# Kernel optimization log

Hardware: AMD Instinct MI355X
Metric: run time of the kernel (lower is better)

Reference implementation:

```python
import jax, jax.numpy as jnp
import numpy as np

HEADS = 16
DIM_HEAD = 64
NPATCH = 256
LN_EPS = 1e-5


def setup_inputs() -> dict:
    key = jax.random.key(0)
    ks = jax.random.split(key, 6)
    B, S, D = 4, 2048, 1024
    inner = HEADS * DIM_HEAD  # 1024
    x = jax.random.normal(ks[0], (B, S, D), dtype=jnp.float32)
    ln_gamma = jnp.ones((D,), dtype=jnp.float32)
    ln_beta = jnp.zeros((D,), dtype=jnp.float32)
    # torch Linear: y = x @ W.T; we store the transposed weight directly.
    Wqkv = jax.random.normal(ks[1], (D, 3 * inner), dtype=jnp.float32) / np.sqrt(D)
    Wout = jax.random.normal(ks[2], (inner, D), dtype=jnp.float32) / np.sqrt(inner)
    bout = jnp.zeros((D,), dtype=jnp.float32)
    return {"x": x, "ln_gamma": ln_gamma, "ln_beta": ln_beta,
            "Wqkv": Wqkv, "Wout": Wout, "bout": bout}


def reference(x, ln_gamma, ln_beta, Wqkv, Wout, bout):
    B, S, D = x.shape
    # LayerNorm
    mu = jnp.mean(x, axis=-1, keepdims=True)
    var = jnp.mean(jnp.square(x - mu), axis=-1, keepdims=True)
    xn = (x - mu) * jax.lax.rsqrt(var + LN_EPS) * ln_gamma + ln_beta
    # QKV projection
    qkv = xn @ Wqkv  # [B, S, 3*H*Dh]
    q, k, v = jnp.split(qkv, 3, axis=-1)
    q = q.reshape(B, S, HEADS, DIM_HEAD)
    k = k.reshape(B, S, HEADS, DIM_HEAD)
    v = v.reshape(B, S, HEADS, DIM_HEAD)
    scale = DIM_HEAD ** -0.5
    dots = jnp.einsum('bqhd,bkhd->bhqk', q, k) * scale  # [B,H,S,S]
    # block-causal mask: query window i attends to key windows 0..i
    win = jnp.arange(S) // NPATCH
    mask = win[:, None] >= win[None, :]  # [S, S] bool
    dots = jnp.where(mask[None, None], dots, -jnp.inf)
    attn = jax.nn.softmax(dots, axis=-1)
    out = jnp.einsum('bhqk,bkhd->bqhd', attn, v).reshape(B, S, HEADS * DIM_HEAD)
    return out @ Wout + bout
```

## Files before the change

### kernel.cpp

```cpp
#include <hip/hip_runtime.h>
#include <stdint.h>

typedef unsigned short u16;
typedef __attribute__((ext_vector_type(8))) short bf16x8;
typedef __attribute__((ext_vector_type(4))) float f32x4;
typedef __attribute__((ext_vector_type(4))) unsigned short u16x4;
typedef __attribute__((ext_vector_type(4))) unsigned int u32x4;

#define DEVI static __device__ __forceinline__

#define QSCALE (0.125f * 1.4426950408889634f)

DEVI u16 f2bf(float f) {
  union { float f; unsigned int u; } v; v.f = f;
  unsigned int u = v.u + 0x7fffu + ((v.u >> 16) & 1u);
  return (u16)(u >> 16);
}
DEVI void gl16(const void* g, void* l) {
  __builtin_amdgcn_global_load_lds(
      (__attribute__((address_space(1))) void*)g,
      (__attribute__((address_space(3))) void*)l, 16, 0, 0);
}
DEVI unsigned int cvtpk(float a, float b) {
  unsigned int r;
  asm("v_cvt_pk_bf16_f32 %0, %1, %2" : "=v"(r) : "v"(a), "v"(b));
  return r;
}
DEVI float fexp2(float x) {
  float r;
  asm("v_exp_f32 %0, %1\n\ts_nop 0" : "=v"(r) : "v"(x));
  return r;
}
DEVI float fmax4(f32x4 v) {
  return fmaxf(fmaxf(v[0], v[1]), fmaxf(v[2], v[3]));
}

__global__ __launch_bounds__(256) void k_ln_split(
    const float* __restrict__ x, const float* __restrict__ gamma,
    const float* __restrict__ beta, u16* __restrict__ xh) {
  const int row = blockIdx.x;
  const int t = threadIdx.x;
  const float4* xr = (const float4*)(x + (size_t)row * 1024);
  float4 v = xr[t];
  float s = v.x + v.y + v.z + v.w;
  float s2 = v.x * v.x + v.y * v.y + v.z * v.z + v.w * v.w;
  #pragma unroll
  for (int m = 1; m < 64; m <<= 1) { s += __shfl_xor(s, m); s2 += __shfl_xor(s2, m); }
  __shared__ float ls[4], ls2[4];
  if ((t & 63) == 0) { ls[t >> 6] = s; ls2[t >> 6] = s2; }
  __syncthreads();
  s = ls[0] + ls[1] + ls[2] + ls[3];
  s2 = ls2[0] + ls2[1] + ls2[2] + ls2[3];
  float mu = s * (1.0f / 1024.0f);
  float var = s2 * (1.0f / 1024.0f) - mu * mu;
  float rstd = rsqrtf(var + 1e-5f);
  float4 g = ((const float4*)gamma)[t];
  float4 b = ((const float4*)beta)[t];
  float xv[4] = {v.x, v.y, v.z, v.w};
  float gg[4] = {g.x, g.y, g.z, g.w};
  float bb[4] = {b.x, b.y, b.z, b.w};
  u16x4 hv;
  #pragma unroll
  for (int i = 0; i < 4; i++) {
    float xn = (xv[i] - mu) * rstd * gg[i] + bb[i];
    hv[i] = f2bf(xn);
  }
  ((u16x4*)xh)[(size_t)row * 256 + t] = hv;
}

__global__ __launch_bounds__(256) void k_wsplit_t(
    const float* __restrict__ W, u16* __restrict__ Wth, int K, int N) {
  __shared__ float tile[32][33];
  const int t = threadIdx.x;
  const int tx = t & 31, ty = t >> 5;
  #pragma unroll
  for (int i = 0; i < 4; i++) {
    int k = blockIdx.y * 32 + ty + i * 8;
    int n = blockIdx.x * 32 + tx;
    tile[ty + i * 8][tx] = W[(size_t)k * N + n];
  }
  __syncthreads();
  #pragma unroll
  for (int i = 0; i < 4; i++) {
    int n = blockIdx.x * 32 + ty + i * 8;
    int k = blockIdx.y * 32 + tx;
    Wth[(size_t)n * K + k] = f2bf(tile[tx][ty + i * 8]);
  }
}

template <int MODE>
__global__ __launch_bounds__(256) void k_gemm(
    const u16* __restrict__ Ah, const u16* __restrict__ Bh,
    u16* __restrict__ Qh, u16* __restrict__ Kh, u16* __restrict__ Vth,
    float* __restrict__ Cout, const float* __restrict__ bias) {
  __shared__ u16 sA[2][128 * 64];
  __shared__ u16 sB[2][128 * 64];
  const int t = threadIdx.x, lane = t & 63, w = t >> 6;
  const int bm = blockIdx.x, bn = blockIdx.y;
  const int wm = (w >> 1) * 64, wn = (w & 1) * 64;
  const int g = lane >> 4, c = lane & 15;
  const size_t arow0 = (size_t)bm * 128, brow0 = (size_t)bn * 128;

  const int r0 = t >> 3, cc0 = t & 7;
  const int cs0 = cc0 ^ (r0 & 7);
  const u16* gA = Ah + (arow0 + r0) * 1024 + cs0 * 8;
  const u16* gB = Bh + (brow0 + r0) * 1024 + cs0 * 8;

  f32x4 acc[4][4] = {};

  #pragma unroll
  for (int i = 0; i < 4; i++) {
    gl16(gA + (size_t)i * 32768, sA[0] + (size_t)(t + i * 256) * 8);
    gl16(gB + (size_t)i * 32768, sB[0] + (size_t)(t + i * 256) * 8);
  }
  gA += 64; gB += 64;
  __syncthreads();

  for (int kt = 0; kt < 16; kt++) {
    const int cur = kt & 1, nxt = cur ^ 1;
    if (kt + 1 < 16) {
      #pragma unroll
      for (int i = 0; i < 4; i++) {
        gl16(gA + (size_t)i * 32768, sA[nxt] + (size_t)(t + i * 256) * 8);
        gl16(gB + (size_t)i * 32768, sB[nxt] + (size_t)(t + i * 256) * 8);
      }
      gA += 64; gB += 64;
    }
    #pragma unroll
    for (int ks = 0; ks < 2; ks++) {
      bf16x8 afh[4], bfh[4];
      #pragma unroll
      for (int mi = 0; mi < 4; mi++) {
        int row = wm + mi * 16 + c;
        afh[mi] = *(const bf16x8*)(sA[cur] + row * 64 + (((ks * 4 + g) ^ (row & 7)) * 8));
      }
      #pragma unroll
      for (int ni = 0; ni < 4; ni++) {
        int row = wn + ni * 16 + c;
        bfh[ni] = *(const bf16x8*)(sB[cur] + row * 64 + (((ks * 4 + g) ^ (row & 7)) * 8));
      }
      #pragma unroll
      for (int mi = 0; mi < 4; mi++)
        #pragma unroll
        for (int ni = 0; ni < 4; ni++)
          acc[mi][ni] = __builtin_amdgcn_mfma_f32_16x16x32_bf16(afh[mi], bfh[ni], acc[mi][ni], 0, 0, 0);
    }
    __syncthreads();
  }

  if (MODE == 0) {
    #pragma unroll
    for (int mi = 0; mi < 4; mi++) {
      int grow0 = bm * 128 + wm + mi * 16 + g * 4;
      int b = grow0 >> 11, s0 = grow0 & 2047;
      #pragma unroll
      for (int ni = 0; ni < 4; ni++) {
        int gcol = bn * 128 + wn + ni * 16 + c;
        int which = gcol >> 10, rem = gcol & 1023;
        int hh = rem >> 6, dd = rem & 63;
        if (which == 2) {
          u16x4 hv;
          #pragma unroll
          for (int r = 0; r < 4; r++) hv[r] = f2bf(acc[mi][ni][r]);
          size_t off = ((size_t)((b * 16 + hh) * 64 + dd)) * 2048 + s0;
          *(u16x4*)(Vth + off) = hv;
        } else {
          u16* dh = which ? Kh : Qh;
          float sc = which ? 1.0f : QSCALE;
          #pragma unroll
          for (int r = 0; r < 4; r++) {
            size_t off = ((size_t)(b * 16 + hh) * 2048 + (s0 + r)) * 64 + dd;
            dh[off] = f2bf(acc[mi][ni][r] * sc);
          }
        }
      }
    }
  } else {
    #pragma unroll
    for (int mi = 0; mi < 4; mi++) {
      int grow0 = bm * 128 + wm + mi * 16 + g * 4;
      #pragma unroll
      for (int ni = 0; ni < 4; ni++) {
        int gcol = bn * 128 + wn + ni * 16 + c;
        float bb = bias[gcol];
        #pragma unroll
        for (int r = 0; r < 4; r++)
          Cout[(size_t)(grow0 + r) * 1024 + gcol] = acc[mi][ni][r] + bb;
      }
    }
  }
}

__global__ __launch_bounds__(512, 4) void k_attn(
    const u16* __restrict__ Qh, const u16* __restrict__ Kh,
    const u16* __restrict__ Vth, u16* __restrict__ Oh) {
  __shared__ u16 lK[2][128 * 64], lV[2][64 * 128];
  const int t = threadIdx.x, lane = t & 63, w = t >> 6;
  const int bh = blockIdx.x;
  const int qt = 15 - blockIdx.y;
  const int b = bh >> 4, h = bh & 15;
  const int qrow0 = qt * 128;
  const int kvlen = (qt / 2 + 1) * 256;
  const int g = lane >> 4, c = lane & 15;

  bf16x8 qf[2];
  {
    const u16* qb = Qh + ((size_t)bh * 2048 + qrow0 + w * 16) * 64;
    #pragma unroll
    for (int ks = 0; ks < 2; ks++)
      qf[ks] = *(const bf16x8*)(qb + (size_t)c * 64 + ks * 32 + g * 8);
  }

  const u16* Kb = Kh + (size_t)bh * 2048 * 64;
  const u16* Vb = Vth + (size_t)bh * 64 * 2048;

  int kbase[2], vbase[4];
  #pragma unroll
  for (int ks = 0; ks < 2; ks++) kbase[ks] = c * 64 + (((ks * 4 + g) ^ (c & 7)) * 8);
  #pragma unroll
  for (int ks = 0; ks < 4; ks++) vbase[ks] = c * 128 + (((ks * 4 + g) ^ c) * 8);

  const int kr0 = t >> 3, kcs0 = (t & 7) ^ (kr0 & 7);
  const int vr0 = t >> 4, vcs0 = (t & 15) ^ (vr0 & 15);

  const bf16x8 vones = {(short)0x3F80, (short)0x3F80, (short)0x3F80, (short)0x3F80,
                        (short)0x3F80, (short)0x3F80, (short)0x3F80, (short)0x3F80};

  float mrun = 0.f;
  f32x4 lsum = {0.f, 0.f, 0.f, 0.f};
  f32x4 o[4] = {};

  const int ntiles = kvlen >> 7;

  gl16(Kb + (size_t)kr0 * 64 + kcs0 * 8, lK[0] + (size_t)t * 8);
  gl16(Kb + (size_t)(kr0 + 64) * 64 + kcs0 * 8, lK[0] + (size_t)(t + 512) * 8);
  gl16(Vb + (size_t)vr0 * 2048 + vcs0 * 8, lV[0] + (size_t)t * 8);
  gl16(Vb + (size_t)(vr0 + 32) * 2048 + vcs0 * 8, lV[0] + (size_t)(t + 512) * 8);
  __syncthreads();

  const u16* gK = Kb + (size_t)(128 + kr0) * 64 + kcs0 * 8;
  const u16* gV = Vb + (size_t)vr0 * 2048 + 128 + vcs0 * 8;

  for (int kt = 0; kt < ntiles; kt++) {
    const int cur = kt & 1, nxt = cur ^ 1;
    if (kt + 1 < ntiles) {
      gl16(gK, lK[nxt] + (size_t)t * 8);
      gl16(gK + 64 * 64, lK[nxt] + (size_t)(t + 512) * 8);
      gl16(gV, lV[nxt] + (size_t)t * 8);
      gl16(gV + 32 * 2048, lV[nxt] + (size_t)(t + 512) * 8);
      gK += 128 * 64;  gV += 128;
    }

    f32x4 s[8];
    #pragma unroll
    for (int ni = 0; ni < 8; ni++)
      s[ni] = (f32x4){-mrun, -mrun, -mrun, -mrun};
    __builtin_amdgcn_s_setprio(1);
    #pragma unroll
    for (int ni = 0; ni < 8; ni++)
      #pragma unroll
      for (int ks = 0; ks < 2; ks++) {
        bf16x8 kf = *(const bf16x8*)(lK[cur] + ni * 1024 + kbase[ks]);
        s[ni] = __builtin_amdgcn_mfma_f32_16x16x32_bf16(kf, qf[ks], s[ni], 0, 0, 0);
      }
    __builtin_amdgcn_s_setprio(0);

    float tl = fmaxf(fmaxf(fmaxf(fmax4(s[0]), fmax4(s[1])), fmaxf(fmax4(s[2]), fmax4(s[3]))),
                     fmaxf(fmaxf(fmax4(s[4]), fmax4(s[5])), fmaxf(fmax4(s[6]), fmax4(s[7]))));
    if (!__all(tl <= 8.0f)) {
      float tm = fmaxf(tl, __shfl_xor(tl, 16));
      tm = fmaxf(tm, __shfl_xor(tm, 32));
      float delta = fmaxf(tm, 0.0f);
      mrun += delta;
      float al = fexp2(-delta);
      #pragma unroll
      for (int ni = 0; ni < 8; ni++)
        #pragma unroll
        for (int r = 0; r < 4; r++) s[ni][r] -= delta;
      #pragma unroll
      for (int r = 0; r < 4; r++) {
        float ar = __shfl(al, g * 4 + r);
        lsum[r] *= ar;
        #pragma unroll
        for (int di = 0; di < 4; di++) o[di][r] *= ar;
      }
    }

    bf16x8 pa[4];
    #pragma unroll
    for (int ks = 0; ks < 4; ks++) {
      unsigned int e0 = cvtpk(fexp2(s[2 * ks][0]), fexp2(s[2 * ks][1]));
      unsigned int e1 = cvtpk(fexp2(s[2 * ks][2]), fexp2(s[2 * ks][3]));
      unsigned int f0 = cvtpk(fexp2(s[2 * ks + 1][0]), fexp2(s[2 * ks + 1][1]));
      unsigned int f1 = cvtpk(fexp2(s[2 * ks + 1][2]), fexp2(s[2 * ks + 1][3]));
      asm volatile("v_permlane32_swap_b32 %0, %1" : "+v"(e0), "+v"(f0));
      asm volatile("v_permlane16_swap_b32 %0, %1" : "+v"(e0), "+v"(f0));
      asm volatile("v_permlane32_swap_b32 %0, %1" : "+v"(e1), "+v"(f1));
      asm volatile("v_permlane16_swap_b32 %0, %1" : "+v"(e1), "+v"(f1));
      union { u32x4 u; bf16x8 bv; } cvu;
      cvu.u = (u32x4){e0, e1, f0, f1};
      pa[ks] = cvu.bv;
    }

    __builtin_amdgcn_s_setprio(1);
    #pragma unroll
    for (int di = 0; di < 4; di++)
      #pragma unroll
      for (int ks = 0; ks < 4; ks++) {
        bf16x8 vf = *(const bf16x8*)(lV[cur] + di * 2048 + vbase[ks]);
        o[di] = __builtin_amdgcn_mfma_f32_16x16x32_bf16(pa[ks], vf, o[di], 0, 0, 0);
      }
    #pragma unroll
    for (int ks = 0; ks < 4; ks++)
      lsum = __builtin_amdgcn_mfma_f32_16x16x32_bf16(pa[ks], vones, lsum, 0, 0, 0);
    __builtin_amdgcn_s_setprio(0);

    __syncthreads();
  }

  #pragma unroll
  for (int r = 0; r < 4; r++) {
    float ir = 1.0f / lsum[r];
    int srow = qrow0 + w * 16 + g * 4 + r;
    size_t rowo = ((size_t)b * 2048 + srow) * 1024 + h * 64;
    #pragma unroll
    for (int di = 0; di < 4; di++)
      Oh[rowo + di * 16 + c] = f2bf(o[di][r] * ir);
  }
}

extern "C" void kernel_launch(void* const* d_in, const int* in_sizes, int n_in,
                              void* d_out, int out_size, void* d_ws, size_t ws_size,
                              hipStream_t stream) {
  const float* x     = (const float*)d_in[0];
  const float* gamma = (const float*)d_in[1];
  const float* beta  = (const float*)d_in[2];
  const float* Wqkv  = (const float*)d_in[3];
  const float* Wout  = (const float*)d_in[4];
  const float* bout  = (const float*)d_in[5];
  float* out = (float*)d_out;

  char* ws = (char*)d_ws;
  size_t off = 0;
  auto alloc = [&](size_t bytes) { char* p = ws + off; off += (bytes + 255) & ~(size_t)255; return p; };
  const size_t SZ_XN = (size_t)8192 * 1024 * 2;
  const size_t SZ_WQ = (size_t)3072 * 1024 * 2;
  const size_t SZ_WO = (size_t)1024 * 1024 * 2;
  const size_t SZ_QKV = (size_t)4 * 16 * 2048 * 64 * 2;
  u16* xnh  = (u16*)alloc(SZ_XN);
  u16* wqth = (u16*)alloc(SZ_WQ);
  u16* woth = (u16*)alloc(SZ_WO);
  u16* Qh  = (u16*)alloc(SZ_QKV);
  u16* Kh  = (u16*)alloc(SZ_QKV);
  u16* Vth = (u16*)alloc(SZ_QKV);
  if (off > ws_size) return;

  k_ln_split<<<8192, 256, 0, stream>>>(x, gamma, beta, xnh);
  k_wsplit_t<<<dim3(96, 32), 256, 0, stream>>>(Wqkv, wqth, 1024, 3072);
  k_wsplit_t<<<dim3(32, 32), 256, 0, stream>>>(Wout, woth, 1024, 1024);
  k_gemm<0><<<dim3(64, 24), 256, 0, stream>>>(xnh, wqth,
                                              Qh, Kh, Vth, nullptr, nullptr);
  k_attn<<<dim3(64, 16), 512, 0, stream>>>(Qh, Kh, Vth, xnh);
  k_gemm<1><<<dim3(64, 8), 256, 0, stream>>>(xnh, woth,
                                             nullptr, nullptr, nullptr,
                                             out, bout);
}
```

Baseline: 164.0 us.

## Use 256x256 tiled, finely pipelined 8-wave GEMM for QKV projection

Replaces the templated 128x128 GEMM for the QKV projection with a dedicated kernel that computes a 256x256 tile using 512 threads (8 waves), each wave holding a 128x64 accumulator. The K loop is split into four sub-phases. Each phase interleaves LDS fragment loads, async global->LDS staging of the next half-tile, and partial vmcnt waits plus barriers, with setprio raised around the MFMA bursts. The goal is more data reuse per loaded tile and better overlap of memory with MFMA. The costs are higher register pressure, 128 KB of LDS per block, and fewer blocks in the grid (384), which may leave some CUs idle. The output projection keeps the old 128x128 kernel, now specialized.

```diff
diff --git a/kernel.cpp b/kernel.cpp
--- a/kernel.cpp
+++ b/kernel.cpp
@@ -88,10 +88,169 @@
   }
 }
 
-template <int MODE>
-__global__ __launch_bounds__(256) void k_gemm(
+__global__ __launch_bounds__(512, 2) void k_gemmq(
     const u16* __restrict__ Ah, const u16* __restrict__ Bh,
-    u16* __restrict__ Qh, u16* __restrict__ Kh, u16* __restrict__ Vth,
+    u16* __restrict__ Qh, u16* __restrict__ Kh, u16* __restrict__ Vth) {
+  __shared__ u16 sA[2][256 * 64];
+  __shared__ u16 sB[2][256 * 64];
+  const int t = threadIdx.x, lane = t & 63, w = t >> 6;
+  const int bm = blockIdx.x, bn = blockIdx.y;
+  const int wm2 = w >> 2, wn4 = w & 3;
+  const int g = lane >> 4, c = lane & 15;
+  const size_t arow0 = (size_t)bm * 256, brow0 = (size_t)bn * 256;
+
+  const int sr = t >> 3;
+  const int scs = (t & 7) ^ (sr & 7);
+  const int brs = (t >> 3) & 31;
+  const int bcs = (t & 7) ^ (brs & 7);
+  const int bsj = t >> 8;
+
+  f32x4 acc[8][4] = {};
+
+#define STAGE_A(u, kt, b) do { \
+    int rA0 = (u) * 64 + sr, rA1 = 128 + rA0; \
+    gl16(Ah + (arow0 + rA0) * 1024 + (size_t)(kt) * 64 + scs * 8, \
+         sA[b] + (size_t)((u) * 512 + t) * 8); \
+    gl16(Ah + (arow0 + rA1) * 1024 + (size_t)(kt) * 64 + scs * 8, \
+         sA[b] + (size_t)(1024 + (u) * 512 + t) * 8); \
+  } while (0)
+#define STAGE_B(u, kt, b) do { \
+    int s0_ = bsj, s1_ = bsj + 2; \
+    int rB0 = (u) * 32 + s0_ * 64 + brs, rB1 = (u) * 32 + s1_ * 64 + brs; \
+    gl16(Bh + (brow0 + rB0) * 1024 + (size_t)(kt) * 64 + bcs * 8, \
+         sB[b] + (size_t)(rB0 * 8 + (t & 7)) * 8); \
+    gl16(Bh + (brow0 + rB1) * 1024 + (size_t)(kt) * 64 + bcs * 8, \
+         sB[b] + (size_t)(rB1 * 8 + (t & 7)) * 8); \
+  } while (0)
+#define PWAIT(tail) do { \
+    if (tail) asm volatile("s_waitcnt vmcnt(0)" ::: "memory"); \
+    else      asm volatile("s_waitcnt vmcnt(6)" ::: "memory"); \
+    __builtin_amdgcn_s_barrier(); \
+    __builtin_amdgcn_sched_barrier(0); \
+  } while (0)
+
+  STAGE_A(0, 0, 0); STAGE_B(0, 0, 0);
+  STAGE_A(1, 0, 0); STAGE_B(1, 0, 0);
+  STAGE_A(0, 1, 1); STAGE_B(0, 1, 1);
+  PWAIT(0);
+
+  bf16x8 af[8], bf0[4], bf1[4];
+  for (int kt = 0; kt < 16; kt++) {
+    const int cur = kt & 1;
+    const int tail = (kt >= 14);
+    const u16* A_ = sA[cur];
+    const u16* B_ = sB[cur];
+
+    #pragma unroll
+    for (int mi = 0; mi < 4; mi++)
+      #pragma unroll
+      for (int ks = 0; ks < 2; ks++) {
+        int row = wm2 * 128 + mi * 16 + c;
+        af[mi * 2 + ks] = *(const bf16x8*)(A_ + row * 64 + (((ks * 4 + g) ^ (row & 7)) * 8));
+      }
+    #pragma unroll
+    for (int ni = 0; ni < 2; ni++)
+      #pragma unroll
+      for (int ks = 0; ks < 2; ks++) {
+        int row = wn4 * 64 + ni * 16 + c;
+        bf0[ni * 2 + ks] = *(const bf16x8*)(B_ + row * 64 + (((ks * 4 + g) ^ (row & 7)) * 8));
+      }
+    if (kt + 1 < 16) STAGE_A(1, kt + 1, (kt + 1) & 1);
+    PWAIT(tail);
+    __builtin_amdgcn_s_setprio(1);
+    #pragma unroll
+    for (int mi = 0; mi < 4; mi++)
+      #pragma unroll
+      for (int ni = 0; ni < 2; ni++)
+        #pragma unroll
+        for (int ks = 0; ks < 2; ks++)
+          acc[mi][ni] = __builtin_amdgcn_mfma_f32_16x16x32_bf16(af[mi * 2 + ks], bf0[ni * 2 + ks], acc[mi][ni], 0, 0, 0);
+    __builtin_amdgcn_s_setprio(0);
+
+    #pragma unroll
+    for (int ni = 0; ni < 2; ni++)
+      #pragma unroll
+      for (int ks = 0; ks < 2; ks++) {
+        int row = wn4 * 64 + 32 + ni * 16 + c;
+        bf1[ni * 2 + ks] = *(const bf16x8*)(B_ + row * 64 + (((ks * 4 + g) ^ (row & 7)) * 8));
+      }
+    if (kt + 1 < 16) STAGE_B(1, kt + 1, (kt + 1) & 1);
+    PWAIT(tail);
+    __builtin_amdgcn_s_setprio(1);
+    #pragma unroll
+    for (int mi = 0; mi < 4; mi++)
+      #pragma unroll
+      for (int ni = 0; ni < 2; ni++)
+        #pragma unroll
+        for (int ks = 0; ks < 2; ks++)
+          acc[mi][2 + ni] = __builtin_amdgcn_mfma_f32_16x16x32_bf16(af[mi * 2 + ks], bf1[ni * 2 + ks], acc[mi][2 + ni], 0, 0, 0);
+    __builtin_amdgcn_s_setprio(0);
+
+    #pragma unroll
+    for (int mi = 0; mi < 4; mi++)
+      #pragma unroll
+      for (int ks = 0; ks < 2; ks++) {
+        int row = wm2 * 128 + 64 + mi * 16 + c;
+        af[mi * 2 + ks] = *(const bf16x8*)(A_ + row * 64 + (((ks * 4 + g) ^ (row & 7)) * 8));
+      }
+    if (kt + 2 < 16) STAGE_A(0, kt + 2, cur);
+    PWAIT(tail);
+    __builtin_amdgcn_s_setprio(1);
+    #pragma unroll
+    for (int mi = 0; mi < 4; mi++)
+      #pragma unroll
+      for (int ni = 0; ni < 2; ni++)
+        #pragma unroll
+        for (int ks = 0; ks < 2; ks++)
+          acc[4 + mi][ni] = __builtin_amdgcn_mfma_f32_16x16x32_bf16(af[mi * 2 + ks], bf0[ni * 2 + ks], acc[4 + mi][ni], 0, 0, 0);
+    __builtin_amdgcn_s_setprio(0);
+
+    if (kt + 2 < 16) STAGE_B(0, kt + 2, cur);
+    PWAIT(tail);
+    __builtin_amdgcn_s_setprio(1);
+    #pragma unroll
+    for (int mi = 0; mi < 4; mi++)
+      #pragma unroll
+      for (int ni = 0; ni < 2; ni++)
+        #pragma unroll
+        for (int ks = 0; ks < 2; ks++)
+          acc[4 + mi][2 + ni] = __builtin_amdgcn_mfma_f32_16x16x32_bf16(af[mi * 2 + ks], bf1[ni * 2 + ks], acc[4 + mi][2 + ni], 0, 0, 0);
+    __builtin_amdgcn_s_setprio(0);
+  }
+
+  #pragma unroll
+  for (int am = 0; am < 8; am++) {
+    int grow0 = bm * 256 + wm2 * 128 + (am >> 2) * 64 + (am & 3) * 16 + g * 4;
+    int b = grow0 >> 11, s0 = grow0 & 2047;
+    #pragma unroll
+    for (int an = 0; an < 4; an++) {
+      int gcol = bn * 256 + wn4 * 64 + (an >> 1) * 32 + (an & 1) * 16 + c;
+      int which = gcol >> 10, rem = gcol & 1023;
+      int hh = rem >> 6, dd = rem & 63;
+      if (which == 2) {
+        u16x4 hv;
+        #pragma unroll
+        for (int r = 0; r < 4; r++) hv[r] = f2bf(acc[am][an][r]);
+        size_t off = ((size_t)((b * 16 + hh) * 64 + dd)) * 2048 + s0;
+        *(u16x4*)(Vth + off) = hv;
+      } else {
+        u16* dh = which ? Kh : Qh;
+        float sc = which ? 1.0f : QSCALE;
+        #pragma unroll
+        for (int r = 0; r < 4; r++) {
+          size_t off = ((size_t)(b * 16 + hh) * 2048 + (s0 + r)) * 64 + dd;
+          dh[off] = f2bf(acc[am][an][r] * sc);
+        }
+      }
+    }
+  }
+#undef STAGE_A
+#undef STAGE_B
+#undef PWAIT
+}
+
+__global__ __launch_bounds__(256) void k_gemmo(
+    const u16* __restrict__ Ah, const u16* __restrict__ Bh,
     float* __restrict__ Cout, const float* __restrict__ bias) {
   __shared__ u16 sA[2][128 * 64];
   __shared__ u16 sB[2][128 * 64];
@@ -148,45 +307,16 @@
     __syncthreads();
   }
 
-  if (MODE == 0) {
-    #pragma unroll
-    for (int mi = 0; mi < 4; mi++) {
-      int grow0 = bm * 128 + wm + mi * 16 + g * 4;
-      int b = grow0 >> 11, s0 = grow0 & 2047;
-      #pragma unroll
-      for (int ni = 0; ni < 4; ni++) {
-        int gcol = bn * 128 + wn + ni * 16 + c;
-        int which = gcol >> 10, rem = gcol & 1023;
-        int hh = rem >> 6, dd = rem & 63;
-        if (which == 2) {
-          u16x4 hv;
-          #pragma unroll
-          for (int r = 0; r < 4; r++) hv[r] = f2bf(acc[mi][ni][r]);
-          size_t off = ((size_t)((b * 16 + hh) * 64 + dd)) * 2048 + s0;
-          *(u16x4*)(Vth + off) = hv;
-        } else {
-          u16* dh = which ? Kh : Qh;
-          float sc = which ? 1.0f : QSCALE;
-          #pragma unroll
-          for (int r = 0; r < 4; r++) {
-            size_t off = ((size_t)(b * 16 + hh) * 2048 + (s0 + r)) * 64 + dd;
-            dh[off] = f2bf(acc[mi][ni][r] * sc);
-          }
-        }
-      }
-    }
-  } else {
-    #pragma unroll
-    for (int mi = 0; mi < 4; mi++) {
-      int grow0 = bm * 128 + wm + mi * 16 + g * 4;
-      #pragma unroll
-      for (int ni = 0; ni < 4; ni++) {
-        int gcol = bn * 128 + wn + ni * 16 + c;
-        float bb = bias[gcol];
-        #pragma unroll
-        for (int r = 0; r < 4; r++)
-          Cout[(size_t)(grow0 + r) * 1024 + gcol] = acc[mi][ni][r] + bb;
-      }
+  #pragma unroll
+  for (int mi = 0; mi < 4; mi++) {
+    int grow0 = bm * 128 + wm + mi * 16 + g * 4;
+    #pragma unroll
+    for (int ni = 0; ni < 4; ni++) {
+      int gcol = bn * 128 + wn + ni * 16 + c;
+      float bb = bias[gcol];
+      #pragma unroll
+      for (int r = 0; r < 4; r++)
+        Cout[(size_t)(grow0 + r) * 1024 + gcol] = acc[mi][ni][r] + bb;
     }
   }
 }
@@ -358,10 +488,7 @@
   k_ln_split<<<8192, 256, 0, stream>>>(x, gamma, beta, xnh);
   k_wsplit_t<<<dim3(96, 32), 256, 0, stream>>>(Wqkv, wqth, 1024, 3072);
   k_wsplit_t<<<dim3(32, 32), 256, 0, stream>>>(Wout, woth, 1024, 1024);
-  k_gemm<0><<<dim3(64, 24), 256, 0, stream>>>(xnh, wqth,
-                                              Qh, Kh, Vth, nullptr, nullptr);
+  k_gemmq<<<dim3(32, 12), 512, 0, stream>>>(xnh, wqth, Qh, Kh, Vth);
   k_attn<<<dim3(64, 16), 512, 0, stream>>>(Qh, Kh, Vth, xnh);
-  k_gemm<1><<<dim3(64, 8), 256, 0, stream>>>(xnh, woth,
-                                             nullptr, nullptr, nullptr,
-                                             out, bout);
-}
+  k_gemmo<<<dim3(64, 8), 256, 0, stream>>>(xnh, woth, out, bout);
+}
```

Result: faster. 158.8 us (-3.2%).
